# Kernel tuning notes

Hardware: AMD Instinct MI355X
Metric: run time of the kernel (lower is better)

The kernel has to match this reference:

```python
import jax, jax.numpy as jnp
import numpy as np
import math

B, S, HID = 4, 2048, 2048
H, KV, D = 16, 4, 128  # heads, kv heads, head_dim; n_rep = H//KV = 4
THETA = 1000000.0


def setup_inputs() -> dict:
    key = jax.random.key(0)
    ks = jax.random.split(key, 6)
    x = jax.random.normal(ks[0], (B, S, HID), dtype=jnp.float32)
    # real RoPE tables (theta=1e6), shape [S, D]
    inv_freq = 1.0 / (THETA ** (jnp.arange(0, D, 2, dtype=jnp.float32) / D))
    t = jnp.arange(S, dtype=jnp.float32)
    freqs = jnp.outer(t, inv_freq)                      # [S, D/2]
    emb = jnp.concatenate([freqs, freqs], axis=-1)      # [S, D]
    cos, sin = jnp.cos(emb), jnp.sin(emb)
    scale = 0.02
    wq = jax.random.normal(ks[1], (H * D, HID), dtype=jnp.float32) * scale
    wk = jax.random.normal(ks[2], (KV * D, HID), dtype=jnp.float32) * scale
    wv = jax.random.normal(ks[3], (KV * D, HID), dtype=jnp.float32) * scale
    wo = jax.random.normal(ks[4], (HID, H * D), dtype=jnp.float32) * scale
    return {"x": x, "cos": cos, "sin": sin, "wq": wq, "wk": wk, "wv": wv, "wo": wo}


def _rotate_half(t):
    half = t.shape[-1] // 2
    return jnp.concatenate([-t[..., half:], t[..., :half]], axis=-1)


def reference(x, cos, sin, wq, wk, wv, wo):
    b, s, _ = x.shape
    rep = H // KV
    # QKV projections (torch Linear: y = x @ W^T)
    q = (x @ wq.T).reshape(b, s, H, D)
    k = (x @ wk.T).reshape(b, s, KV, D)
    v = (x @ wv.T).reshape(b, s, KV, D)
    # RoPE, cos/sin broadcast over batch and heads: [1, S, 1, D]
    c = cos[None, :s, None, :]
    si = sin[None, :s, None, :]
    q = q * c + _rotate_half(q) * si
    k = k * c + _rotate_half(k) * si
    # GQA without materializing repeated KV: group q heads as [KV, rep]
    qg = q.reshape(b, s, KV, rep, D)
    scale = 1.0 / math.sqrt(D)
    # flash path in source: SDPA with default is_causal=False -> full (non-causal) attention
    scores = jnp.einsum('bqkrd,bskd->bkrqs', qg, k) * scale  # [B, KV, rep, S, S]
    attn = jax.nn.softmax(scores, axis=-1)
    out = jnp.einsum('bkrqs,bskd->bqkrd', attn, v).reshape(b, s, H * D)
    return out @ wo.T
```

## Files before the change

kernel.cpp:

```cpp
#include <hip/hip_runtime.h>
#include <stdint.h>

#define BB 4
#define SS 2048
#define HIDW 2048
#define NH 16
#define NKV 4
#define DD 128

typedef unsigned short u16;
typedef unsigned long long u64;
typedef unsigned int uint;
typedef __attribute__((ext_vector_type(8))) short bf16x8;
typedef __attribute__((ext_vector_type(4))) float f32x4;
typedef __attribute__((ext_vector_type(2))) float f32x2;
typedef __attribute__((ext_vector_type(2))) __bf16 bf16x2;

__device__ __forceinline__ u16 f2bf1(float f) {
  __bf16 h = (__bf16)f;
  return __builtin_bit_cast(u16, h);
}

__device__ __forceinline__ float bf2f(u16 v) {
  return __uint_as_float((uint)v << 16);
}

__device__ __forceinline__ uint pkbf(float a, float b) {
  f32x2 v = {a, b};
  bf16x2 h = __builtin_convertvector(v, bf16x2);
  return __builtin_bit_cast(uint, h);
}

__device__ __forceinline__ void gld_lds16(const void* g, void* s) {
  __builtin_amdgcn_global_load_lds(
      (const __attribute__((address_space(1))) void*)g,
      (__attribute__((address_space(3))) void*)(unsigned)(uintptr_t)s,
      16, 0, 0);
}

__global__ __launch_bounds__(256) void cast_f32_bf16(const float* __restrict__ in,
                                                     u16* __restrict__ out, int n4) {
  int i = blockIdx.x * 256 + threadIdx.x;
  if (i < n4) {
    float4 f = ((const float4*)in)[i];
    uint2 o;
    o.x = pkbf(f.x, f.y);
    o.y = pkbf(f.z, f.w);
    ((uint2*)out)[i] = o;
  }
}

__global__ __launch_bounds__(256) void cast_weights(const float* __restrict__ wq,
                                                    const float* __restrict__ wk,
                                                    const float* __restrict__ wv,
                                                    const float* __restrict__ wo,
                                                    u16* __restrict__ wqkvb,
                                                    u16* __restrict__ wob) {
  int i = blockIdx.x * 256 + threadIdx.x;
  const float* src;
  uint2* dst;
  int off;
  if (i < 1048576) {
    src = wq; dst = (uint2*)wqkvb; off = i;
  } else if (i < 1310720) {
    src = wk; dst = (uint2*)(wqkvb + (size_t)2048 * 2048); off = i - 1048576;
  } else if (i < 1572864) {
    src = wv; dst = (uint2*)(wqkvb + (size_t)2560 * 2048); off = i - 1310720;
  } else {
    src = wo; dst = (uint2*)wob; off = i - 1572864;
  }
  float4 f = ((const float4*)src)[off];
  uint2 o;
  o.x = pkbf(f.x, f.y);
  o.y = pkbf(f.z, f.w);
  dst[off] = o;
}

__global__ __launch_bounds__(256) void gemm_bt(const u16* __restrict__ A,
                                               const u16* __restrict__ Bt,
                                               float* __restrict__ C,
                                               int M, int N, int K) {
  __shared__ u16 As[128 * 32];
  __shared__ u16 Bs[128 * 32];
  const int tid = threadIdx.x;
  const int wave = tid >> 6, lane = tid & 63;
  const int lr = lane & 15, lq = lane >> 4;
  const int row0 = blockIdx.y * 128, col0 = blockIdx.x * 128;
  const int wm = (wave >> 1) * 64, wn = (wave & 1) * 64;

  const int trow = tid >> 2;
  const int tblk = (tid & 3) ^ (trow & 3);
  const u16* aSrc = A + (size_t)(row0 + trow) * K + tblk * 8;
  const u16* bSrc = Bt + (size_t)(col0 + trow) * K + tblk * 8;
  char* ldsA = (char*)As + wave * 1024;
  char* ldsB = (char*)Bs + wave * 1024;

  f32x4 acc[4][4] = {};
  const int aoff = (wm + lr) * 32 + ((lq ^ (lr & 3)) * 8);
  const int boff = (wn + lr) * 32 + ((lq ^ (lr & 3)) * 8);

  for (int k0 = 0; k0 < K; k0 += 32) {
    __syncthreads();
    gld_lds16(aSrc + k0, ldsA);
    gld_lds16(aSrc + (size_t)64 * K + k0, ldsA + 4096);
    gld_lds16(bSrc + k0, ldsB);
    gld_lds16(bSrc + (size_t)64 * K + k0, ldsB + 4096);
    __syncthreads();
    bf16x8 a[4], b[4];
#pragma unroll
    for (int i = 0; i < 4; i++) a[i] = *(const bf16x8*)(As + aoff + i * 512);
#pragma unroll
    for (int j = 0; j < 4; j++) b[j] = *(const bf16x8*)(Bs + boff + j * 512);
#pragma unroll
    for (int i = 0; i < 4; i++)
#pragma unroll
      for (int j = 0; j < 4; j++)
        acc[i][j] = __builtin_amdgcn_mfma_f32_16x16x32_bf16(a[i], b[j], acc[i][j], 0, 0, 0);
  }
#pragma unroll
  for (int i = 0; i < 4; i++) {
    int row = row0 + wm + i * 16 + lq * 4;
#pragma unroll
    for (int j = 0; j < 4; j++) {
      int col = col0 + wn + j * 16 + lr;
      float* cp = C + (size_t)row * N + col;
#pragma unroll
      for (int r = 0; r < 4; r++) cp[(size_t)r * N] = acc[i][j][r];
    }
  }
}

__global__ __launch_bounds__(256) void gemm_qkv_rope(const u16* __restrict__ A,
                                                     const u16* __restrict__ Bt,
                                                     const float* __restrict__ cosT,
                                                     const float* __restrict__ sinT,
                                                     u16* __restrict__ qb,
                                                     u16* __restrict__ kb,
                                                     u16* __restrict__ vt) {
  __shared__ u16 As[128 * 32];
  __shared__ u16 Bs[128 * 32];
  const int tid = threadIdx.x;
  const int wave = tid >> 6, lane = tid & 63;
  const int lr = lane & 15, lq = lane >> 4;
  const int row0 = blockIdx.y * 128, col0 = blockIdx.x * 128;
  const int K = HIDW;

  const int trow = tid >> 2;
  const int tblk = (tid & 3) ^ (trow & 3);
  const u16* aSrc = A + (size_t)(row0 + trow) * K + tblk * 8;
  const u16* bSrc = Bt + (size_t)(col0 + trow) * K + tblk * 8;
  char* ldsA = (char*)As + wave * 1024;
  char* ldsB = (char*)Bs + wave * 1024;

  f32x4 acc[2][8] = {};
  const int aoff = (wave * 32 + lr) * 32 + ((lq ^ (lr & 3)) * 8);
  const int boff = lr * 32 + ((lq ^ (lr & 3)) * 8);

  for (int k0 = 0; k0 < K; k0 += 32) {
    __syncthreads();
    gld_lds16(aSrc + k0, ldsA);
    gld_lds16(aSrc + (size_t)64 * K + k0, ldsA + 4096);
    gld_lds16(bSrc + k0, ldsB);
    gld_lds16(bSrc + (size_t)64 * K + k0, ldsB + 4096);
    __syncthreads();
    bf16x8 a[2], b[8];
#pragma unroll
    for (int i = 0; i < 2; i++) a[i] = *(const bf16x8*)(As + aoff + i * 512);
#pragma unroll
    for (int j = 0; j < 8; j++) b[j] = *(const bf16x8*)(Bs + boff + j * 512);
#pragma unroll
    for (int i = 0; i < 2; i++)
#pragma unroll
      for (int j = 0; j < 8; j++)
        acc[i][j] = __builtin_amdgcn_mfma_f32_16x16x32_bf16(a[i], b[j], acc[i][j], 0, 0, 0);
  }

  const int b_ = row0 >> 11;
  const int s_base = (row0 & (SS - 1)) + wave * 32;
  const int hsel = col0 >> 7;

  if (hsel < 20) {
    const float scale = (hsel < 16) ? 0.08838834764831845f : 1.0f;
    u16* base = (hsel < 16)
                    ? qb + (size_t)(b_ * NH + hsel) * SS * DD
                    : kb + (size_t)(b_ * NKV + (hsel - 16)) * SS * DD;
#pragma unroll
    for (int i = 0; i < 2; i++) {
#pragma unroll
      for (int r = 0; r < 4; r++) {
        int s = s_base + i * 16 + lq * 4 + r;
        const float* cp = cosT + (size_t)s * DD;
        const float* sp = sinT + (size_t)s * DD;
        u16* drow = base + (size_t)s * DD;
#pragma unroll
        for (int j = 0; j < 4; j++) {
          int d = j * 16 + lr;
          float c = cp[d], si = sp[d];
          float x0 = acc[i][j][r] * scale, x1 = acc[i][j + 4][r] * scale;
          drow[d] = f2bf1(x0 * c - x1 * si);
          drow[d + 64] = f2bf1(x1 * c + x0 * si);
        }
      }
    }
  } else {
    const int kv = hsel - 20;
#pragma unroll
    for (int i = 0; i < 2; i++) {
      int s = s_base + i * 16 + lq * 4;
#pragma unroll
      for (int j = 0; j < 8; j++) {
        int d = j * 16 + lr;
        u64 pw = (u64)pkbf(acc[i][j][0], acc[i][j][1]) |
                 ((u64)pkbf(acc[i][j][2], acc[i][j][3]) << 32);
        *(u64*)(vt + (size_t)((b_ * NKV + kv) * DD + d) * SS + s) = pw;
      }
    }
  }
}

__global__ __launch_bounds__(256, 2) void flash_attn(const u16* __restrict__ qb,
                                                     const u16* __restrict__ kb,
                                                     const u16* __restrict__ vt,
                                                     u16* __restrict__ ob) {
  __shared__ u16 Ks[2][64 * 128];
  __shared__ u16 Vs[2][128 * 64];
  __shared__ u16 Pt[128 * 64];
  const int tid = threadIdx.x;
  const int wave = tid >> 6, lane = tid & 63;
  const int lr = lane & 15, lq = lane >> 4;

  const int lin = blockIdx.y * 16 + blockIdx.x;
  const int xcd = lin & 7;
  const int slot = lin >> 3;
  const int pr = xcd + ((slot & 1) << 3);
  const int b = pr >> 2, kvh = pr & 3;
  const int rest = slot >> 1;
  const int h = kvh * 4 + (rest & 3);
  const int q0 = (rest >> 2) * 128;
  const int bh = b * 16 + h;

  const size_t kbase = (size_t)(b * NKV + kvh) * SS * DD;
  const size_t vbase = (size_t)(b * NKV + kvh) * DD * SS;

  bf16x8 qf[2][4];
#pragma unroll
  for (int nt = 0; nt < 2; nt++) {
    const u16* qrow = qb + ((size_t)bh * SS + q0 + wave * 32 + nt * 16 + lr) * DD + lq * 8;
#pragma unroll
    for (int kk = 0; kk < 4; kk++) qf[nt][kk] = *(const bf16x8*)(qrow + kk * 32);
  }

  f32x4 o_acc[8][2] = {};
  float l_i[2] = {0.0f, 0.0f};

  const int ktrow = tid >> 4;
  const int ktblk = (tid & 15) ^ ktrow;
  const u16* ksrc = kb + kbase + (size_t)ktrow * DD + ktblk * 8;
  const int vtrow = tid >> 3;
  const int vtblk = (tid & 7) ^ (vtrow & 7);
  const u16* vsrc = vt + vbase + (size_t)vtrow * SS + vtblk * 8;

  {
    char* kd = (char*)(Ks[0]) + wave * 1024;
    char* vd = (char*)(Vs[0]) + wave * 1024;
#pragma unroll
    for (int c = 0; c < 4; c++) {
      gld_lds16(ksrc + (size_t)c * 16 * DD, kd + c * 4096);
      gld_lds16(vsrc + (size_t)c * 32 * SS, vd + c * 4096);
    }
  }

  for (int it = 0; it < SS / 64; it++) {
    __syncthreads();
    if (it + 1 < SS / 64) {
      int s0 = (it + 1) * 64;
      char* kd = (char*)(Ks[(it + 1) & 1]) + wave * 1024;
      char* vd = (char*)(Vs[(it + 1) & 1]) + wave * 1024;
#pragma unroll
      for (int c = 0; c < 4; c++) {
        gld_lds16(ksrc + (size_t)(s0 + c * 16) * DD, kd + c * 4096);
        gld_lds16(vsrc + s0 + (size_t)c * 32 * SS, vd + c * 4096);
      }
    }
    const u16* K = Ks[it & 1];
    const u16* V = Vs[it & 1];

    f32x4 sc[4][2] = {};
#pragma unroll
    for (int kk = 0; kk < 4; kk++) {
#pragma unroll
      for (int mt = 0; mt < 4; mt++) {
        bf16x8 kf = *(const bf16x8*)(K + (mt * 16 + lr) * 128 + (((kk * 4 + lq) ^ lr) * 8));
#pragma unroll
        for (int nt = 0; nt < 2; nt++)
          sc[mt][nt] = __builtin_amdgcn_mfma_f32_16x16x32_bf16(kf, qf[nt][kk], sc[mt][nt], 0, 0, 0);
      }
    }

#pragma unroll
    for (int nt = 0; nt < 2; nt++) {
      float rs = 0.0f;
#pragma unroll
      for (int mt = 0; mt < 4; mt++)
#pragma unroll
        for (int r = 0; r < 4; r++) {
          float p = __expf(sc[mt][nt][r]);
          sc[mt][nt][r] = p;
          rs += p;
        }
      l_i[nt] += rs;
      int prow = wave * 32 + nt * 16 + lr;
#pragma unroll
      for (int mt = 0; mt < 4; mt++) {
        u64 pw = (u64)pkbf(sc[mt][nt][0], sc[mt][nt][1]) |
                 ((u64)pkbf(sc[mt][nt][2], sc[mt][nt][3]) << 32);
        int bb = (mt * 2 + (lq >> 1)) ^ (lr & 7);
        *(u64*)((char*)Pt + prow * 128 + bb * 16 + (lq & 1) * 8) = pw;
      }
    }

#pragma unroll
    for (int kk2 = 0; kk2 < 2; kk2++) {
      bf16x8 pbf[2];
#pragma unroll
      for (int nt = 0; nt < 2; nt++) {
        int prow = wave * 32 + nt * 16 + lr;
        pbf[nt] = *(const bf16x8*)((char*)Pt + prow * 128 + (((kk2 * 4 + lq) ^ (lr & 7)) * 16));
      }
#pragma unroll
      for (int mt = 0; mt < 8; mt++) {
        bf16x8 vf = *(const bf16x8*)(V + (mt * 16 + lr) * 64 + (((kk2 * 4 + lq) ^ (lr & 7)) * 8));
#pragma unroll
        for (int nt = 0; nt < 2; nt++)
          o_acc[mt][nt] = __builtin_amdgcn_mfma_f32_16x16x32_bf16(vf, pbf[nt], o_acc[mt][nt], 0, 0, 0);
      }
    }
  }

#pragma unroll
  for (int nt = 0; nt < 2; nt++) {
    float l = l_i[nt];
    l += __shfl_xor(l, 16, 64);
    l += __shfl_xor(l, 32, 64);
    float inv = 1.0f / l;
    size_t q = (size_t)q0 + wave * 32 + nt * 16 + lr;
    u16* dst = ob + ((size_t)b * SS + q) * HIDW + h * DD + lq * 4;
#pragma unroll
    for (int mt = 0; mt < 8; mt++) {
      uint2 pk;
      pk.x = pkbf(o_acc[mt][nt][0] * inv, o_acc[mt][nt][1] * inv);
      pk.y = pkbf(o_acc[mt][nt][2] * inv, o_acc[mt][nt][3] * inv);
      *(uint2*)(dst + mt * 16) = pk;
    }
  }
}

extern "C" void kernel_launch(void* const* d_in, const int* in_sizes, int n_in,
                              void* d_out, int out_size, void* d_ws, size_t ws_size,
                              hipStream_t stream) {
  const float* x = (const float*)d_in[0];
  const float* cosT = (const float*)d_in[1];
  const float* sinT = (const float*)d_in[2];
  const float* wq = (const float*)d_in[3];
  const float* wk = (const float*)d_in[4];
  const float* wv = (const float*)d_in[5];
  const float* wo = (const float*)d_in[6];
  float* out = (float*)d_out;

  char* ws = (char*)d_ws;
  size_t off = 0;
  auto alloc = [&](size_t bytes) {
    char* p = ws + off;
    off += (bytes + 255) & ~(size_t)255;
    return p;
  };
  const int M = BB * SS;
  u16* xb = (u16*)alloc((size_t)M * HIDW * 2);
  u16* wqkvb = (u16*)alloc((size_t)3072 * HIDW * 2);
  u16* wob = (u16*)alloc((size_t)HIDW * NH * DD * 2);
  u16* qb = (u16*)alloc((size_t)BB * NH * SS * DD * 2);
  u16* kb = (u16*)alloc((size_t)BB * NKV * SS * DD * 2);
  u16* vt = (u16*)alloc((size_t)BB * NKV * DD * SS * 2);
  u16* ob = (u16*)alloc((size_t)M * HIDW * 2);

  cast_f32_bf16<<<(M * HIDW) / 1024, 256, 0, stream>>>(x, xb, (M * HIDW) / 4);
  cast_weights<<<10240, 256, 0, stream>>>(wq, wk, wv, wo, wqkvb, wob);

  gemm_qkv_rope<<<dim3(3072 / 128, M / 128), 256, 0, stream>>>(xb, wqkvb, cosT, sinT,
                                                               qb, kb, vt);

  flash_attn<<<dim3(SS / 128, BB * NH), 256, 0, stream>>>(qb, kb, vt, ob);

  gemm_bt<<<dim3(HIDW / 128, M / 128), 256, 0, stream>>>(ob, wob, out, M, HIDW, NH * DD);
}
```

Baseline: 526.1 us.

## Replace QKV and output GEMMs with 256x256 double-buffered pipelined tiles

Swaps the 128x128, single-buffered GEMM kernels for a shared 256x256-tile, 512-thread mainloop. It uses a K-step of 64, double-buffered LDS filled by async global-to-LDS loads with explicit vmcnt waits, loads interleaved with MFMA phases, and raised priority around the MFMA blocks. Blocks are remapped so that neighbouring tiles land on the same XCD. The aim is more data reuse per tile and hiding load latency behind MFMA. The cost is 128KB of LDS per block and heavy register use, which limits occupancy, plus fragile hand-ordered barriers.

```diff
diff --git a/kernel.cpp b/kernel.cpp
--- a/kernel.cpp
+++ b/kernel.cpp
@@ -36,6 +36,14 @@
       (const __attribute__((address_space(1))) void*)g,
       (__attribute__((address_space(3))) void*)(unsigned)(uintptr_t)s,
       16, 0, 0);
+}
+
+#define VMCNT(n) asm volatile("s_waitcnt vmcnt(" #n ")" ::: "memory")
+
+__device__ __forceinline__ void barx() {
+  asm volatile("" ::: "memory");
+  __builtin_amdgcn_s_barrier();
+  asm volatile("" ::: "memory");
 }
 
 __global__ __launch_bounds__(256) void cast_f32_bf16(const float* __restrict__ in,
@@ -76,108 +84,155 @@
   dst[off] = o;
 }
 
-__global__ __launch_bounds__(256) void gemm_bt(const u16* __restrict__ A,
-                                               const u16* __restrict__ Bt,
-                                               float* __restrict__ C,
-                                               int M, int N, int K) {
-  __shared__ u16 As[128 * 32];
-  __shared__ u16 Bs[128 * 32];
+__device__ __forceinline__ void mm256(const u16* __restrict__ A,
+                                      const u16* __restrict__ Bt,
+                                      int row0, int col0, f32x4 (&acc)[4][8]) {
+  __shared__ u16 S[2][2][16384];
   const int tid = threadIdx.x;
   const int wave = tid >> 6, lane = tid & 63;
   const int lr = lane & 15, lq = lane >> 4;
-  const int row0 = blockIdx.y * 128, col0 = blockIdx.x * 128;
-  const int wm = (wave >> 1) * 64, wn = (wave & 1) * 64;
-
-  const int trow = tid >> 2;
-  const int tblk = (tid & 3) ^ (trow & 3);
-  const u16* aSrc = A + (size_t)(row0 + trow) * K + tblk * 8;
-  const u16* bSrc = Bt + (size_t)(col0 + trow) * K + tblk * 8;
-  char* ldsA = (char*)As + wave * 1024;
-  char* ldsB = (char*)Bs + wave * 1024;
-
-  f32x4 acc[4][4] = {};
-  const int aoff = (wm + lr) * 32 + ((lq ^ (lr & 3)) * 8);
-  const int boff = (wn + lr) * 32 + ((lq ^ (lr & 3)) * 8);
-
-  for (int k0 = 0; k0 < K; k0 += 32) {
-    __syncthreads();
-    gld_lds16(aSrc + k0, ldsA);
-    gld_lds16(aSrc + (size_t)64 * K + k0, ldsA + 4096);
-    gld_lds16(bSrc + k0, ldsB);
-    gld_lds16(bSrc + (size_t)64 * K + k0, ldsB + 4096);
-    __syncthreads();
-    bf16x8 a[4], b[4];
-#pragma unroll
-    for (int i = 0; i < 4; i++) a[i] = *(const bf16x8*)(As + aoff + i * 512);
-#pragma unroll
-    for (int j = 0; j < 4; j++) b[j] = *(const bf16x8*)(Bs + boff + j * 512);
-#pragma unroll
-    for (int i = 0; i < 4; i++)
-#pragma unroll
-      for (int j = 0; j < 4; j++)
-        acc[i][j] = __builtin_amdgcn_mfma_f32_16x16x32_bf16(a[i], b[j], acc[i][j], 0, 0, 0);
-  }
-#pragma unroll
-  for (int i = 0; i < 4; i++) {
-    int row = row0 + wm + i * 16 + lq * 4;
-#pragma unroll
-    for (int j = 0; j < 4; j++) {
-      int col = col0 + wn + j * 16 + lr;
-      float* cp = C + (size_t)row * N + col;
-#pragma unroll
-      for (int r = 0; r < 4; r++) cp[(size_t)r * N] = acc[i][j][r];
-    }
-  }
-}
-
-__global__ __launch_bounds__(256) void gemm_qkv_rope(const u16* __restrict__ A,
-                                                     const u16* __restrict__ Bt,
-                                                     const float* __restrict__ cosT,
-                                                     const float* __restrict__ sinT,
-                                                     u16* __restrict__ qb,
-                                                     u16* __restrict__ kb,
-                                                     u16* __restrict__ vt) {
-  __shared__ u16 As[128 * 32];
-  __shared__ u16 Bs[128 * 32];
+  const int wr = wave >> 1, wc = wave & 1;
+
+  const int sk = ((tid & 7) * 8) ^ (((tid >> 5) & 1) << 4);
+  const u16* aS = A + (size_t)(row0 + (tid >> 3)) * 2048 + sk;
+  const u16* bS = Bt + (size_t)(col0 + (tid >> 3)) * 2048 + sk;
+
+  const int rsw = (lq * 16) ^ (((lr >> 2) & 1) << 5);
+  const int aoff = (wr * 64 + lr) * 128 + rsw;
+  const int boff = (wc * 128 + lr) * 128 + rsw;
+
+  auto stA = [&](int buf, int h, int k0) {
+    char* d = (char*)&S[buf][0][0] + h * 16384 + wave * 1024;
+    const u16* s = aS + (size_t)h * 262144 + k0;
+    gld_lds16(s, d);
+    gld_lds16(s + 131072, d + 8192);
+  };
+  auto stB = [&](int buf, int h, int k0) {
+    char* d = (char*)&S[buf][1][0] + h * 16384 + wave * 1024;
+    const u16* s = bS + (size_t)h * 262144 + k0;
+    gld_lds16(s, d);
+    gld_lds16(s + 131072, d + 8192);
+  };
+
+  stA(0, 0, 0);
+  stA(0, 1, 0);
+  stB(0, 0, 0);
+  stB(0, 1, 0);
+
+  for (int t = 0; t < 32; ++t) {
+    const int cur = t & 1;
+    const char* LA = (const char*)&S[cur][0][0];
+    const char* LB = (const char*)&S[cur][1][0];
+    const int nk0 = (t + 1) * 64;
+
+    if (t < 31) {
+      stA(cur ^ 1, 0, nk0);
+      stA(cur ^ 1, 1, nk0);
+      VMCNT(4);
+    } else {
+      VMCNT(0);
+    }
+    barx();
+
+    bf16x8 a0[2][2], a1[2][2], bq[4][2];
+#pragma unroll
+    for (int m2 = 0; m2 < 2; ++m2)
+#pragma unroll
+      for (int kk = 0; kk < 2; ++kk)
+        a0[m2][kk] = *(const bf16x8*)(LA + aoff + m2 * 2048 + kk * 64);
+#pragma unroll
+    for (int n = 0; n < 4; ++n)
+#pragma unroll
+      for (int kk = 0; kk < 2; ++kk)
+        bq[n][kk] = *(const bf16x8*)(LB + boff + n * 2048 + kk * 64);
+    if (t < 31) stB(cur ^ 1, 0, nk0);
+    barx();
+    __builtin_amdgcn_s_setprio(1);
+#pragma unroll
+    for (int kk = 0; kk < 2; ++kk)
+#pragma unroll
+      for (int m2 = 0; m2 < 2; ++m2)
+#pragma unroll
+        for (int n = 0; n < 4; ++n)
+          acc[m2][n] = __builtin_amdgcn_mfma_f32_16x16x32_bf16(a0[m2][kk], bq[n][kk],
+                                                               acc[m2][n], 0, 0, 0);
+    __builtin_amdgcn_s_setprio(0);
+    barx();
+
+#pragma unroll
+    for (int m2 = 0; m2 < 2; ++m2)
+#pragma unroll
+      for (int kk = 0; kk < 2; ++kk)
+        a1[m2][kk] = *(const bf16x8*)(LA + aoff + (m2 + 2) * 2048 + kk * 64);
+    if (t < 31) stB(cur ^ 1, 1, nk0);
+    barx();
+    __builtin_amdgcn_s_setprio(1);
+#pragma unroll
+    for (int kk = 0; kk < 2; ++kk)
+#pragma unroll
+      for (int m2 = 0; m2 < 2; ++m2)
+#pragma unroll
+        for (int n = 0; n < 4; ++n)
+          acc[m2 + 2][n] = __builtin_amdgcn_mfma_f32_16x16x32_bf16(a1[m2][kk], bq[n][kk],
+                                                                   acc[m2 + 2][n], 0, 0, 0);
+    __builtin_amdgcn_s_setprio(0);
+    barx();
+
+#pragma unroll
+    for (int n = 0; n < 4; ++n)
+#pragma unroll
+      for (int kk = 0; kk < 2; ++kk)
+        bq[n][kk] = *(const bf16x8*)(LB + boff + (n + 4) * 2048 + kk * 64);
+    barx();
+    __builtin_amdgcn_s_setprio(1);
+#pragma unroll
+    for (int kk = 0; kk < 2; ++kk)
+#pragma unroll
+      for (int m2 = 0; m2 < 2; ++m2)
+#pragma unroll
+        for (int n = 0; n < 4; ++n)
+          acc[m2 + 2][n + 4] = __builtin_amdgcn_mfma_f32_16x16x32_bf16(
+              a1[m2][kk], bq[n][kk], acc[m2 + 2][n + 4], 0, 0, 0);
+    __builtin_amdgcn_s_setprio(0);
+    barx();
+
+    __builtin_amdgcn_s_setprio(1);
+#pragma unroll
+    for (int kk = 0; kk < 2; ++kk)
+#pragma unroll
+      for (int m2 = 0; m2 < 2; ++m2)
+#pragma unroll
+        for (int n = 0; n < 4; ++n)
+          acc[m2][n + 4] = __builtin_amdgcn_mfma_f32_16x16x32_bf16(
+              a0[m2][kk], bq[n][kk], acc[m2][n + 4], 0, 0, 0);
+    __builtin_amdgcn_s_setprio(0);
+    barx();
+  }
+}
+
+__global__ __launch_bounds__(512, 2) void gemm_qkv_rope256(const u16* __restrict__ A,
+                                                           const u16* __restrict__ Bt,
+                                                           const float* __restrict__ cosT,
+                                                           const float* __restrict__ sinT,
+                                                           u16* __restrict__ qb,
+                                                           u16* __restrict__ kb,
+                                                           u16* __restrict__ vt) {
+  const int bid = blockIdx.x;
+  const int nid = (bid & 7) * 48 + (bid >> 3);
+  const int bxx = nid % 12, byy = nid / 12;
+  const int row0 = byy * 256, col0 = bxx * 256;
+
+  f32x4 acc[4][8] = {};
+  mm256(A, Bt, row0, col0, acc);
+
   const int tid = threadIdx.x;
   const int wave = tid >> 6, lane = tid & 63;
   const int lr = lane & 15, lq = lane >> 4;
-  const int row0 = blockIdx.y * 128, col0 = blockIdx.x * 128;
-  const int K = HIDW;
-
-  const int trow = tid >> 2;
-  const int tblk = (tid & 3) ^ (trow & 3);
-  const u16* aSrc = A + (size_t)(row0 + trow) * K + tblk * 8;
-  const u16* bSrc = Bt + (size_t)(col0 + trow) * K + tblk * 8;
-  char* ldsA = (char*)As + wave * 1024;
-  char* ldsB = (char*)Bs + wave * 1024;
-
-  f32x4 acc[2][8] = {};
-  const int aoff = (wave * 32 + lr) * 32 + ((lq ^ (lr & 3)) * 8);
-  const int boff = lr * 32 + ((lq ^ (lr & 3)) * 8);
-
-  for (int k0 = 0; k0 < K; k0 += 32) {
-    __syncthreads();
-    gld_lds16(aSrc + k0, ldsA);
-    gld_lds16(aSrc + (size_t)64 * K + k0, ldsA + 4096);
-    gld_lds16(bSrc + k0, ldsB);
-    gld_lds16(bSrc + (size_t)64 * K + k0, ldsB + 4096);
-    __syncthreads();
-    bf16x8 a[2], b[8];
-#pragma unroll
-    for (int i = 0; i < 2; i++) a[i] = *(const bf16x8*)(As + aoff + i * 512);
-#pragma unroll
-    for (int j = 0; j < 8; j++) b[j] = *(const bf16x8*)(Bs + boff + j * 512);
-#pragma unroll
-    for (int i = 0; i < 2; i++)
-#pragma unroll
-      for (int j = 0; j < 8; j++)
-        acc[i][j] = __builtin_amdgcn_mfma_f32_16x16x32_bf16(a[i], b[j], acc[i][j], 0, 0, 0);
-  }
+  const int wr = wave >> 1, wc = wave & 1;
 
   const int b_ = row0 >> 11;
-  const int s_base = (row0 & (SS - 1)) + wave * 32;
-  const int hsel = col0 >> 7;
+  const int sbase = (row0 & (SS - 1)) + wr * 64;
+  const int hsel = bxx * 2 + wc;
 
   if (hsel < 20) {
     const float scale = (hsel < 16) ? 0.08838834764831845f : 1.0f;
@@ -185,10 +240,10 @@
                     ? qb + (size_t)(b_ * NH + hsel) * SS * DD
                     : kb + (size_t)(b_ * NKV + (hsel - 16)) * SS * DD;
 #pragma unroll
-    for (int i = 0; i < 2; i++) {
+    for (int i = 0; i < 4; i++) {
 #pragma unroll
       for (int r = 0; r < 4; r++) {
-        int s = s_base + i * 16 + lq * 4 + r;
+        int s = sbase + i * 16 + lq * 4 + r;
         const float* cp = cosT + (size_t)s * DD;
         const float* sp = sinT + (size_t)s * DD;
         u16* drow = base + (size_t)s * DD;
@@ -205,8 +260,8 @@
   } else {
     const int kv = hsel - 20;
 #pragma unroll
-    for (int i = 0; i < 2; i++) {
-      int s = s_base + i * 16 + lq * 4;
+    for (int i = 0; i < 4; i++) {
+      int s = sbase + i * 16 + lq * 4;
 #pragma unroll
       for (int j = 0; j < 8; j++) {
         int d = j * 16 + lr;
@@ -214,6 +269,35 @@
                  ((u64)pkbf(acc[i][j][2], acc[i][j][3]) << 32);
         *(u64*)(vt + (size_t)((b_ * NKV + kv) * DD + d) * SS + s) = pw;
       }
+    }
+  }
+}
+
+__global__ __launch_bounds__(512, 2) void gemm_out256(const u16* __restrict__ A,
+                                                      const u16* __restrict__ Bt,
+                                                      float* __restrict__ C) {
+  const int bid = blockIdx.x;
+  const int nid = (bid & 7) * 32 + (bid >> 3);
+  const int bxx = nid & 7, byy = nid >> 3;
+  const int row0 = byy * 256, col0 = bxx * 256;
+
+  f32x4 acc[4][8] = {};
+  mm256(A, Bt, row0, col0, acc);
+
+  const int tid = threadIdx.x;
+  const int wave = tid >> 6, lane = tid & 63;
+  const int lr = lane & 15, lq = lane >> 4;
+  const int wr = wave >> 1, wc = wave & 1;
+
+#pragma unroll
+  for (int i = 0; i < 4; i++) {
+    int row = row0 + wr * 64 + i * 16 + lq * 4;
+#pragma unroll
+    for (int j = 0; j < 8; j++) {
+      int col = col0 + wc * 128 + j * 16 + lr;
+      float* cp = C + (size_t)row * HIDW + col;
+#pragma unroll
+      for (int r = 0; r < 4; r++) cp[(size_t)r * HIDW] = acc[i][j][r];
     }
   }
 }
@@ -386,10 +470,9 @@
   cast_f32_bf16<<<(M * HIDW) / 1024, 256, 0, stream>>>(x, xb, (M * HIDW) / 4);
   cast_weights<<<10240, 256, 0, stream>>>(wq, wk, wv, wo, wqkvb, wob);
 
-  gemm_qkv_rope<<<dim3(3072 / 128, M / 128), 256, 0, stream>>>(xb, wqkvb, cosT, sinT,
-                                                               qb, kb, vt);
+  gemm_qkv_rope256<<<384, 512, 0, stream>>>(xb, wqkvb, cosT, sinT, qb, kb, vt);
 
   flash_attn<<<dim3(SS / 128, BB * NH), 256, 0, stream>>>(qb, kb, vt, ob);
 
-  gemm_bt<<<dim3(HIDW / 128, M / 128), 256, 0, stream>>>(ob, wob, out, M, HIDW, NH * DD);
-}
+  gemm_out256<<<256, 512, 0, stream>>>(ob, wob, out);
+}
```

Result: faster. 494.2 us (-6.1%).
